# Optimization experiments

Measured on AMD Instinct MI355X. Metric: run time of the kernel, lower is better.

## Reference

```python
import jax, jax.numpy as jnp
import numpy as np

B, T, H, L = 64, 64, 256, 2
INPUT_SIZE = 65
E = INPUT_SIZE - 1  # encoder_in


def setup_inputs() -> dict:
    key = jax.random.key(0)
    ks = jax.random.split(key, 20)
    s = 0.05
    p = {}
    p["input_data"] = jax.random.normal(ks[0], (B, T, INPUT_SIZE), jnp.float32)
    # encoder LSTM (input E -> H, L layers; torch gate order i,f,g,o)
    p["w_ih_e0"] = jax.random.normal(ks[1], (4 * H, E), jnp.float32) * s
    p["w_ih_e1"] = jax.random.normal(ks[2], (L - 1, 4 * H, H), jnp.float32) * s
    p["w_hh_e"] = jax.random.normal(ks[3], (L, 4 * H, H), jnp.float32) * s
    p["b_ih_e"] = jax.random.normal(ks[4], (L, 4 * H), jnp.float32) * s
    p["b_hh_e"] = jax.random.normal(ks[5], (L, 4 * H), jnp.float32) * s
    # decoder LSTM (input H+1 -> H, L layers)
    p["w_ih_d0"] = jax.random.normal(ks[6], (4 * H, H + 1), jnp.float32) * s
    p["w_ih_d1"] = jax.random.normal(ks[7], (L - 1, 4 * H, H), jnp.float32) * s
    p["w_hh_d"] = jax.random.normal(ks[8], (L, 4 * H, H), jnp.float32) * s
    p["b_ih_d"] = jax.random.normal(ks[9], (L, 4 * H), jnp.float32) * s
    p["b_hh_d"] = jax.random.normal(ks[10], (L, 4 * H), jnp.float32) * s
    # encoder attention MLP: Linear(2H+T -> E), Tanh, Linear(E -> 1, no bias)
    p["attn_w1"] = jax.random.normal(ks[11], (E, 2 * H + T), jnp.float32) * s
    p["attn_b1"] = jax.random.normal(ks[12], (E,), jnp.float32) * s
    p["attn_w2"] = jax.random.normal(ks[13], (E,), jnp.float32) * s
    # decoder attention MLP: Linear(3H -> H), Tanh, Linear(H -> 1, no bias)
    p["attnd_w1"] = jax.random.normal(ks[14], (H, 3 * H), jnp.float32) * s
    p["attnd_b1"] = jax.random.normal(ks[15], (H,), jnp.float32) * s
    p["attnd_w2"] = jax.random.normal(ks[16], (H,), jnp.float32) * s
    # output projection: Linear(2H -> 1)
    p["proj_w"] = jax.random.normal(ks[17], (1, 2 * H), jnp.float32) * s
    p["proj_b"] = jax.random.normal(ks[18], (1,), jnp.float32) * s
    return p


def _lstm_step(x, h, c, w_ih0, w_ih_rest, w_hh, b_ih, b_hh):
    """Single-timestep multi-layer LSTM. x: [B, in], h/c: [L, B, H]."""
    hs, cs = [], []
    inp = x
    for l in range(L):
        w_ih = w_ih0 if l == 0 else w_ih_rest[l - 1]
        gates = inp @ w_ih.T + b_ih[l] + h[l] @ w_hh[l].T + b_hh[l]  # [B, 4H]
        i, f, g, o = jnp.split(gates, 4, axis=-1)
        c_new = jax.nn.sigmoid(f) * c[l] + jax.nn.sigmoid(i) * jnp.tanh(g)
        h_new = jax.nn.sigmoid(o) * jnp.tanh(c_new)
        hs.append(h_new)
        cs.append(c_new)
        inp = h_new
    return jnp.stack(hs), jnp.stack(cs)


def reference(input_data, w_ih_e0, w_ih_e1, w_hh_e, b_ih_e, b_hh_e,
              w_ih_d0, w_ih_d1, w_hh_d, b_ih_d, b_hh_d,
              attn_w1, attn_b1, attn_w2, attnd_w1, attnd_b1, attnd_w2,
              proj_w, proj_b):
    input_encoder = input_data[:, :, 1:]             # [B, T, E]
    input_decoder = input_data[:, :, 0]              # [B, T]
    input_permuted = jnp.transpose(input_encoder, (0, 2, 1))  # [B, E, T]

    h0 = jnp.zeros((L, B, H), input_data.dtype)
    c0 = jnp.zeros((L, B, H), input_data.dtype)

    def enc_step(carry, x_t):  # x_t: [B, E]
        h, c = carry
        feat = jnp.concatenate([
            jnp.broadcast_to(h[-1][:, None, :], (B, E, H)),
            jnp.broadcast_to(c[-1][:, None, :], (B, E, H)),
            input_permuted], axis=-1)                # [B, E, 2H+T]
        z = jnp.tanh(feat @ attn_w1.T + attn_b1)     # [B, E, E]
        a = jax.nn.softmax(z @ attn_w2, axis=-1)     # [B, E]
        h, c = _lstm_step(x_t * a, h, c, w_ih_e0, w_ih_e1, w_hh_e, b_ih_e, b_hh_e)
        return (h, c), h[-1]

    _, h_tops = jax.lax.scan(enc_step, (h0, c0), jnp.transpose(input_encoder, (1, 0, 2)))
    h_expanded = jnp.transpose(h_tops, (1, 0, 2))    # [B, T, H]

    def dec_step(carry, d_t):  # d_t: [B]
        h, c = carry
        feat = jnp.concatenate([
            jnp.broadcast_to(h[-1][:, None, :], (B, T, H)),
            jnp.broadcast_to(c[-1][:, None, :], (B, T, H)),
            h_expanded], axis=-1)                    # [B, T, 3H]
        z = jnp.tanh(feat @ attnd_w1.T + attnd_b1)   # [B, T, H]
        a = jax.nn.softmax(z @ attnd_w2, axis=-1)    # [B, T]
        partial = jnp.einsum('bth,bt->bh', h_expanded, a)  # [B, H]
        full = jnp.concatenate([partial, d_t[:, None]], axis=-1)  # [B, H+1]
        h, c = _lstm_step(full, h, c, w_ih_d0, w_ih_d1, w_hh_d, b_ih_d, b_hh_d)
        return (h, c), partial

    (h_d, c_d), partials = jax.lax.scan(dec_step, (h0, c0), input_decoder.T)
    out = jnp.abs(jnp.concatenate([h_d[-1], partials[-1]], axis=-1) @ proj_w.T + proj_b)  # [B, 1]
    return out
```

## Files before the change

### kernel.cpp

```cpp
#include <hip/hip_runtime.h>
#include <hip/hip_fp16.h>
#include <math.h>

#define NT 1024

typedef _Float16 h2v __attribute__((ext_vector_type(2)));
union H8 { uint4 u; h2v h[4]; };

__device__ __forceinline__ float sigf(float x)   { return 1.0f / (1.0f + __expf(-x)); }
__device__ __forceinline__ float tanhf_(float x) { return 1.0f - 2.0f / (1.0f + __expf(2.0f * x)); }
__device__ __forceinline__ float dot4(float4 a, float4 b) {
    return a.x * b.x + a.y * b.y + a.z * b.z + a.w * b.w;
}
__device__ __forceinline__ float red16(float v) {
    v += __shfl_xor(v, 1); v += __shfl_xor(v, 2);
    v += __shfl_xor(v, 4); v += __shfl_xor(v, 8);
    return v;
}
__device__ __forceinline__ float red64(float v) {
    v += __shfl_xor(v, 1);  v += __shfl_xor(v, 2);  v += __shfl_xor(v, 4);
    v += __shfl_xor(v, 8);  v += __shfl_xor(v, 16); v += __shfl_xor(v, 32);
    return v;
}
__device__ __forceinline__ float dot2h(h2v a, h2v b, float c) {
#if __has_builtin(__builtin_amdgcn_fdot2)
    return __builtin_amdgcn_fdot2(a, b, c, false);
#else
    return c + (float)a[0] * (float)b[0] + (float)a[1] * (float)b[1];
#endif
}

__device__ __forceinline__ float exr(const float* p) {
    return __hip_atomic_load(p, __ATOMIC_RELAXED, __HIP_MEMORY_SCOPE_AGENT);
}

__device__ __forceinline__ void xbar(unsigned* ctr, unsigned target) {
    asm volatile("s_waitcnt vmcnt(0)" ::: "memory");
    __syncthreads();
    if (threadIdx.x == 0) {
        __hip_atomic_fetch_add(ctr, 1u, __ATOMIC_RELAXED, __HIP_MEMORY_SCOPE_AGENT);
        while (__hip_atomic_load(ctr, __ATOMIC_RELAXED, __HIP_MEMORY_SCOPE_AGENT) < target)
            __builtin_amdgcn_s_sleep(1);
    }
    __syncthreads();
}

#define OFF_RA   0
#define OFF_RE0  32768
#define OFF_RE1  425984
#define OFF_RDW1 950272
#define OFF_RD0  1081344
#define OFF_RDT  1605632
#define OFF_RD1  1606656
#define TOT_H    2130944

template<int ITERS, bool BIAS, bool DT>
__device__ __forceinline__ void gemv512x(const __half* __restrict__ W,
                                         const __half* __restrict__ act,
                                         const float* __restrict__ bias,
                                         const __half* __restrict__ rdt, float dts,
                                         float* __restrict__ outg,
                                         int jBase, int ljBase) {
    const int lane = threadIdx.x & 63;
    const int q = lane & 15, g = lane >> 4;
    H8 a0, a1, a2, a3;
    a0.u = *(const uint4*)(act + 8 * q);
    a1.u = *(const uint4*)(act + 8 * q + 128);
    a2.u = *(const uint4*)(act + 8 * q + 256);
    a3.u = *(const uint4*)(act + 8 * q + 384);
    #pragma unroll 2
    for (int it = 0; it < ITERS; ++it) {
        const int j = jBase + it * 4 + g;
        const uint4* wp = (const uint4*)(W + ((size_t)j << 9) + 32 * q);
        H8 w0, w1, w2, w3;
        w0.u = wp[0]; w1.u = wp[1]; w2.u = wp[2]; w3.u = wp[3];
        float s0 = 0.f, s1 = 0.f;
        #pragma unroll
        for (int i = 0; i < 4; ++i) {
            s0 = dot2h(w0.h[i], a0.h[i], s0);
            s1 = dot2h(w1.h[i], a1.h[i], s1);
            s0 = dot2h(w2.h[i], a2.h[i], s0);
            s1 = dot2h(w3.h[i], a3.h[i], s1);
        }
        float s = s0 + s1;
        s += __shfl_xor(s, 1); s += __shfl_xor(s, 2);
        s += __shfl_xor(s, 4); s += __shfl_xor(s, 8);
        if (q == 0) {
            if (DT) s += dts * (float)rdt[j];
            outg[ljBase + it * 4 + g] = BIAS ? s + bias[j] : s;
        }
    }
}

template<int ITERS>
__device__ __forceinline__ void gemv384x(const __half* __restrict__ W,
                                         const __half* __restrict__ act,
                                         const float* __restrict__ bias,
                                         float* __restrict__ outg,
                                         int jBase, int ljBase) {
    const int lane = threadIdx.x & 63;
    const int q = lane & 15, g = lane >> 4;
    H8 a0, a1, a2;
    a0.u = *(const uint4*)(act + 8 * q);
    a1.u = *(const uint4*)(act + 8 * q + 128);
    a2.u = *(const uint4*)(act + 8 * q + 256);
    #pragma unroll 2
    for (int it = 0; it < ITERS; ++it) {
        const int j = jBase + it * 4 + g;
        const uint4* wp = (const uint4*)(W + (size_t)j * 384 + 24 * q);
        H8 w0, w1, w2;
        w0.u = wp[0]; w1.u = wp[1]; w2.u = wp[2];
        float s0 = 0.f, s1 = 0.f;
        #pragma unroll
        for (int i = 0; i < 4; ++i) {
            s0 = dot2h(w0.h[i], a0.h[i], s0);
            s1 = dot2h(w1.h[i], a1.h[i], s1);
            s0 = dot2h(w2.h[i], a2.h[i], s0);
        }
        float s = s0 + s1;
        s += __shfl_xor(s, 1); s += __shfl_xor(s, 2);
        s += __shfl_xor(s, 4); s += __shfl_xor(s, 8);
        if (q == 0) outg[ljBase + it * 4 + g] = s + bias[j];
    }
}

#define M_HEXP  0
#define M_XET   16384
#define M_GSL   20736
#define M_HCT   20992
#define M_TMP   21248
#define M_SCORE 21312
#define M_AS    21376
#define M_C0    21440
#define M_C1    21504
#define M_HC1F  21568
#define M_DECIN 21824
#define M_PARTF 21888
#define M_BE0   22144
#define M_BE1   23168
#define M_BD0   24192
#define M_BD1   25216
#define M_AHC   26240
#define M_AE0   26496
#define M_AHH   26688
#define M_AD0   26944
#define M_RDT   27200
#define M_TOT   27712

extern "C" __global__ void __launch_bounds__(NT)
attn_lstm_v6(const float* __restrict__ inp,  const __half* __restrict__ wsh,
             float* __restrict__ h0x, float* __restrict__ h1x,
             float* __restrict__ hcx, unsigned* __restrict__ barc,
             const float* __restrict__ bihe, const float* __restrict__ bhhe,
             const float* __restrict__ bihd, const float* __restrict__ bhhd,
             const float* __restrict__ aw1,  const float* __restrict__ ab1,
             const float* __restrict__ aw2,
             const float* __restrict__ dw1,  const float* __restrict__ db1,
             const float* __restrict__ dw2,
             const float* __restrict__ pw,   const float* __restrict__ pb,
             float* __restrict__ out)
{
    extern __shared__ __align__(16) float sm[];
    float* hexp   = sm + M_HEXP;
    float* xeT    = sm + M_XET;
    float* gsl    = sm + M_GSL;
    float* hctL   = sm + M_HCT;
    float* tmp64  = sm + M_TMP;
    float* scoreS = sm + M_SCORE;
    float* aS     = sm + M_AS;
    float* c0L    = sm + M_C0;
    float* c1L    = sm + M_C1;
    float* hc1f   = sm + M_HC1F;
    float* decin  = sm + M_DECIN;
    float* partF  = sm + M_PARTF;
    float* bE0    = sm + M_BE0;
    float* bE1    = sm + M_BE1;
    float* bD0    = sm + M_BD0;
    float* bD1    = sm + M_BD1;
    __half* aHC   = (__half*)(sm + M_AHC);
    __half* aE0   = (__half*)(sm + M_AE0);
    __half* aHH   = (__half*)(sm + M_AHH);
    __half* aD0   = (__half*)(sm + M_AD0);
    __half* rdtL  = (__half*)(sm + M_RDT);

    const __half* RA   = wsh + OFF_RA;
    const __half* RE0  = wsh + OFF_RE0;
    const __half* RE1  = wsh + OFF_RE1;
    const __half* RDW1 = wsh + OFF_RDW1;
    const __half* RD0  = wsh + OFF_RD0;
    const __half* RD1  = wsh + OFF_RD1;

    const int tid = threadIdx.x;
    const int b   = blockIdx.x >> 2;
    const int co  = blockIdx.x & 3;
    const int w   = tid >> 6;
    unsigned* ctr = barc + (b << 4);
    unsigned  ph  = 0;

    if (tid < 64) { c0L[tid] = 0.f; c1L[tid] = 0.f; }
    for (int i = tid; i < 960; i += NT) sm[M_AHC + i] = 0.0f;
    if (tid < 512) sm[M_RDT + tid] = ((const float*)(wsh + OFF_RDT))[tid];
    {
        int j = tid;
        bE0[j] = bihe[j]        + bhhe[j];
        bE1[j] = bihe[1024 + j] + bhhe[1024 + j];
        bD0[j] = bihd[j]        + bhhd[j];
        bD1[j] = bihd[1024 + j] + bhhd[1024 + j];
    }
    const float* ib = inp + b * (64 * 65);
    for (int i = tid; i < 4096; i += NT) {
        int t = i & 63, e = i >> 6;
        xeT[e * 68 + t] = ib[t * 65 + 1 + e];
    }
    if (tid < 64) decin[tid] = ib[tid * 65];
    __syncthreads();

    const int g16 = tid >> 4, q16 = tid & 15;
    const int gg = w >> 2, cb = (w & 3) << 4;
    const int jB  = gg * 256 + co * 64 + cb;
    const int ljB = gg * 64 + cb;

    float Preg[4], w2r[4];
    #pragma unroll
    for (int jj = 0; jj < 4; ++jj) {
        int j = q16 + 16 * jj;
        w2r[jj] = aw2[j];
        float acc = ab1[j];
        const float4* w4 = (const float4*)(aw1 + j * 576 + 512);
        const float4* x4 = (const float4*)(xeT + g16 * 68);
        #pragma unroll 4
        for (int k = 0; k < 16; ++k) acc += dot4(w4[k], x4[k]);
        Preg[jj] = acc;
    }

    for (int t = 0; t < 64; ++t) {
        const int p = t & 1;
        float* h0b = h0x + p * 16384 + b * 256;
        float* h1b = h1x + p * 32768 + b * 512;
        gemv512x<1, false, false>(RA, aHC, nullptr, nullptr, 0.f, hctL, w * 4, w * 4);
        __syncthreads();
        {
            float s = 0.f;
            #pragma unroll
            for (int jj = 0; jj < 4; ++jj)
                s += tanhf_(Preg[jj] + hctL[q16 + 16 * jj]) * w2r[jj];
            s = red16(s);
            if (q16 == 0) scoreS[g16] = s;
        }
        __syncthreads();
        if (tid < 64) {
            float v = scoreS[tid], m = v;
            #pragma unroll
            for (int d = 1; d < 64; d <<= 1) m = fmaxf(m, __shfl_xor(m, d));
            float ex = __expf(v - m), s = ex;
            #pragma unroll
            for (int d = 1; d < 64; d <<= 1) s += __shfl_xor(s, d);
            aE0[tid] = __float2half((ex / s) * xeT[tid * 68 + t]);
        }
        __syncthreads();
        gemv384x<4>(RE0, aE0, bE0, gsl, jB, ljB);
        __syncthreads();
        if (tid < 64) {
            float cn = sigf(gsl[64 + tid]) * c0L[tid] + sigf(gsl[tid]) * tanhf_(gsl[128 + tid]);
            float hn = sigf(gsl[192 + tid]) * tanhf_(cn);
            c0L[tid] = cn;
            atomicExch(&h0b[co * 64 + tid], hn);
        }
        xbar(ctr, ++ph * 4u);
        if (tid < 256) {
            __half hh = __float2half(exr(&h0b[tid]));
            aE0[64 + tid] = hh; aHH[tid] = hh;
        }
        __syncthreads();
        gemv512x<4, true, false>(RE1, aHH, bE1, nullptr, 0.f, gsl, jB, ljB);
        __syncthreads();
        if (tid < 64) {
            float cn = sigf(gsl[64 + tid]) * c1L[tid] + sigf(gsl[tid]) * tanhf_(gsl[128 + tid]);
            float hn = sigf(gsl[192 + tid]) * tanhf_(cn);
            c1L[tid] = cn;
            atomicExch(&h1b[co * 64 + tid], hn);
            atomicExch(&h1b[256 + co * 64 + tid], cn);
        }
        xbar(ctr, ++ph * 4u);
        if (tid < 512) {
            float v = exr(&h1b[tid]);
            __half hh = __float2half(v);
            aHC[tid] = hh;
            if (tid < 256) { aHH[256 + tid] = hh; hexp[t * 256 + tid] = v; }
        }
        __syncthreads();
    }

    if (tid < 64) { c0L[tid] = 0.f; c1L[tid] = 0.f; }
    for (int i = tid; i < 960; i += NT) sm[M_AHC + i] = 0.0f;
    __syncthreads();
    float Pdreg[16], w2dr[16];
    #pragma unroll
    for (int jj = 0; jj < 16; ++jj) {
        int j = q16 + 16 * jj;
        w2dr[jj] = dw2[j];
        float acc = db1[j];
        const float4* w4 = (const float4*)(dw1 + j * 768 + 512);
        const float4* x4 = (const float4*)(hexp + g16 * 256);
        #pragma unroll 4
        for (int k = 0; k < 64; ++k) acc += dot4(w4[k], x4[k]);
        Pdreg[jj] = acc;
    }
    __syncthreads();

    const int j4 = tid >> 2, q4 = tid & 3;
    for (int t = 0; t < 64; ++t) {
        const int p = t & 1;
        float* h0b = h0x + p * 16384 + b * 256;
        float* h1b = h1x + p * 32768 + b * 512;
        float* hcb = hcx + p * 16384 + b * 256;
        gemv512x<1, false, false>(RDW1, aHC, nullptr, nullptr, 0.f, tmp64,
                                  co * 64 + w * 4, w * 4);
        __syncthreads();
        if (tid < 64) atomicExch(&hcb[co * 64 + tid], tmp64[tid]);
        xbar(ctr, ++ph * 4u);
        if (tid < 256) hctL[tid] = exr(&hcb[tid]);
        __syncthreads();
        {
            float s = 0.f;
            #pragma unroll
            for (int jj = 0; jj < 16; ++jj)
                s += tanhf_(Pdreg[jj] + hctL[q16 + 16 * jj]) * w2dr[jj];
            s = red16(s);
            if (q16 == 0) scoreS[g16] = s;
        }
        __syncthreads();
        if (tid < 64) {
            float v = scoreS[tid], m = v;
            #pragma unroll
            for (int d = 1; d < 64; d <<= 1) m = fmaxf(m, __shfl_xor(m, d));
            float ex = __expf(v - m), s = ex;
            #pragma unroll
            for (int d = 1; d < 64; d <<= 1) s += __shfl_xor(s, d);
            aS[tid] = ex / s;
        }
        __syncthreads();
        {
            float acc = 0.f;
            #pragma unroll 4
            for (int i = 0; i < 16; ++i) {
                int tt = q4 + 4 * i;
                acc += hexp[tt * 256 + j4] * aS[tt];
            }
            acc += __shfl_xor(acc, 1);
            acc += __shfl_xor(acc, 2);
            if (q4 == 0) { aD0[j4] = __float2half(acc); partF[j4] = acc; }
        }
        __syncthreads();
        gemv512x<4, true, true>(RD0, aD0, bD0, rdtL, decin[t], gsl, jB, ljB);
        __syncthreads();
        if (tid < 64) {
            float cn = sigf(gsl[64 + tid]) * c0L[tid] + sigf(gsl[tid]) * tanhf_(gsl[128 + tid]);
            float hn = sigf(gsl[192 + tid]) * tanhf_(cn);
            c0L[tid] = cn;
            atomicExch(&h0b[co * 64 + tid], hn);
        }
        xbar(ctr, ++ph * 4u);
        if (tid < 256) {
            __half hh = __float2half(exr(&h0b[tid]));
            aD0[256 + tid] = hh; aHH[tid] = hh;
        }
        __syncthreads();
        gemv512x<4, true, false>(RD1, aHH, bD1, nullptr, 0.f, gsl, jB, ljB);
        __syncthreads();
        if (tid < 64) {
            float cn = sigf(gsl[64 + tid]) * c1L[tid] + sigf(gsl[tid]) * tanhf_(gsl[128 + tid]);
            float hn = sigf(gsl[192 + tid]) * tanhf_(cn);
            c1L[tid] = cn;
            atomicExch(&h1b[co * 64 + tid], hn);
            atomicExch(&h1b[256 + co * 64 + tid], cn);
        }
        xbar(ctr, ++ph * 4u);
        if (tid < 512) {
            float v = exr(&h1b[tid]);
            __half hh = __float2half(v);
            aHC[tid] = hh;
            if (tid < 256) { aHH[256 + tid] = hh; hc1f[tid] = v; }
        }
        __syncthreads();
    }

    if (co == 0 && tid < 64) {
        float acc = 0.f;
        #pragma unroll
        for (int i = 0; i < 8; ++i) {
            int k = tid + 64 * i;
            float v = (k < 256) ? hc1f[k] : partF[k - 256];
            acc += v * pw[k];
        }
        acc = red64(acc);
        if (tid == 0) out[b] = fabsf(acc + pb[0]);
    }
}

#define L_HEXP   0
#define L_XET    16384
#define L_GSL    20736
#define L_HCT    21760
#define L_SCORE  22016
#define L_AS     22080
#define L_C0     22144
#define L_HC1F   22400
#define L_DECIN  22912
#define L_PARTF  22976
#define L_BE0    23232
#define L_BE1    24256
#define L_BD0    25280
#define L_BD1    26304
#define L_AHC    27328
#define L_AE0    27584
#define L_AHH    27776
#define L_AD0    28032
#define L_RDT    28288
#define L_TOT    28800

extern "C" __global__ void __launch_bounds__(NT)
attn_lstm_v5(const float* __restrict__ inp,  const __half* __restrict__ wsh,
             const float* __restrict__ bihe, const float* __restrict__ bhhe,
             const float* __restrict__ bihd, const float* __restrict__ bhhd,
             const float* __restrict__ aw1,  const float* __restrict__ ab1,
             const float* __restrict__ aw2,
             const float* __restrict__ dw1,  const float* __restrict__ db1,
             const float* __restrict__ dw2,
             const float* __restrict__ pw,   const float* __restrict__ pb,
             float* __restrict__ out)
{
    extern __shared__ __align__(16) float sm[];
    float* hexp   = sm + L_HEXP;
    float* xeT    = sm + L_XET;
    float* gsl    = sm + L_GSL;
    float* hctL   = sm + L_HCT;
    float* scoreS = sm + L_SCORE;
    float* aS     = sm + L_AS;
    float* c0L    = sm + L_C0;
    float* hc1f   = sm + L_HC1F;
    float* decin  = sm + L_DECIN;
    float* partF  = sm + L_PARTF;
    float* bE0    = sm + L_BE0;
    float* bE1    = sm + L_BE1;
    float* bD0    = sm + L_BD0;
    float* bD1    = sm + L_BD1;
    __half* aHC   = (__half*)(sm + L_AHC);
    __half* aE0   = (__half*)(sm + L_AE0);
    __half* aHH   = (__half*)(sm + L_AHH);
    __half* aD0   = (__half*)(sm + L_AD0);
    __half* rdtL  = (__half*)(sm + L_RDT);

    const __half* RA   = wsh + OFF_RA;
    const __half* RE0  = wsh + OFF_RE0;
    const __half* RE1  = wsh + OFF_RE1;
    const __half* RDW1 = wsh + OFF_RDW1;
    const __half* RD0  = wsh + OFF_RD0;
    const __half* RD1  = wsh + OFF_RD1;

    const int b   = blockIdx.x;
    const int tid = threadIdx.x;
    const int w   = tid >> 6;

    for (int i = tid; i < (L_BE0 - L_C0); i += NT) sm[L_C0 + i] = 0.0f;
    for (int i = tid; i < (L_RDT - L_AHC); i += NT) sm[L_AHC + i] = 0.0f;
    if (tid < 512) sm[L_RDT + tid] = ((const float*)(wsh + OFF_RDT))[tid];
    {
        int j = tid;
        bE0[j] = bihe[j]        + bhhe[j];
        bE1[j] = bihe[1024 + j] + bhhe[1024 + j];
        bD0[j] = bihd[j]        + bhhd[j];
        bD1[j] = bihd[1024 + j] + bhhd[1024 + j];
    }
    const float* ib = inp + b * (64 * 65);
    for (int i = tid; i < 4096; i += NT) {
        int t = i & 63, e = i >> 6;
        xeT[e * 68 + t] = ib[t * 65 + 1 + e];
    }
    if (tid < 64) decin[tid] = ib[tid * 65];
    __syncthreads();

    const int g16 = tid >> 4, q16 = tid & 15;

    float Preg[4], w2r[4];
    #pragma unroll
    for (int jj = 0; jj < 4; ++jj) {
        int j = q16 + 16 * jj;
        w2r[jj] = aw2[j];
        float acc = ab1[j];
        const float4* w4 = (const float4*)(aw1 + j * 576 + 512);
        const float4* x4 = (const float4*)(xeT + g16 * 68);
        #pragma unroll 4
        for (int k = 0; k < 16; ++k) acc += dot4(w4[k], x4[k]);
        Preg[jj] = acc;
    }

    for (int t = 0; t < 64; ++t) {
        gemv512x<1, false, false>(RA, aHC, nullptr, nullptr, 0.f, hctL, w * 4, w * 4);
        __syncthreads();
        {
            float s = 0.f;
            #pragma unroll
            for (int jj = 0; jj < 4; ++jj)
                s += tanhf_(Preg[jj] + hctL[q16 + 16 * jj]) * w2r[jj];
            s = red16(s);
            if (q16 == 0) scoreS[g16] = s;
        }
        __syncthreads();
        if (tid < 64) {
            float v = scoreS[tid], m = v;
            #pragma unroll
            for (int d = 1; d < 64; d <<= 1) m = fmaxf(m, __shfl_xor(m, d));
            float ex = __expf(v - m), s = ex;
            #pragma unroll
            for (int d = 1; d < 64; d <<= 1) s += __shfl_xor(s, d);
            aE0[tid] = __float2half((ex / s) * xeT[tid * 68 + t]);
        }
        __syncthreads();
        gemv384x<16>(RE0, aE0, bE0, gsl, w * 64, w * 64);
        __syncthreads();
        if (tid < 256) {
            float cn = sigf(gsl[256 + tid]) * c0L[tid] + sigf(gsl[tid]) * tanhf_(gsl[512 + tid]);
            float hn = sigf(gsl[768 + tid]) * tanhf_(cn);
            c0L[tid] = cn;
            __half hh = __float2half(hn);
            aE0[64 + tid] = hh; aHH[tid] = hh;
        }
        __syncthreads();
        gemv512x<16, true, false>(RE1, aHH, bE1, nullptr, 0.f, gsl, w * 64, w * 64);
        __syncthreads();
        if (tid < 256) {
            float cp = hc1f[256 + tid];
            float cn = sigf(gsl[256 + tid]) * cp + sigf(gsl[tid]) * tanhf_(gsl[512 + tid]);
            float hn = sigf(gsl[768 + tid]) * tanhf_(cn);
            hc1f[tid] = hn; hc1f[256 + tid] = cn;
            __half hh = __float2half(hn);
            aHC[tid] = hh; aHC[256 + tid] = __float2half(cn);
            aHH[256 + tid] = hh;
            hexp[t * 256 + tid] = hn;
        }
        __syncthreads();
    }

    if (tid < 256) { c0L[tid] = 0.0f; hc1f[tid] = 0.0f; hc1f[256 + tid] = 0.0f; }
    for (int i = tid; i < (L_RDT - L_AHC); i += NT) sm[L_AHC + i] = 0.0f;
    __syncthreads();
    float Pdreg[16], w2dr[16];
    #pragma unroll
    for (int jj = 0; jj < 16; ++jj) {
        int j = q16 + 16 * jj;
        w2dr[jj] = dw2[j];
        float acc = db1[j];
        const float4* w4 = (const float4*)(dw1 + j * 768 + 512);
        const float4* x4 = (const float4*)(hexp + g16 * 256);
        #pragma unroll 4
        for (int k = 0; k < 64; ++k) acc += dot4(w4[k], x4[k]);
        Pdreg[jj] = acc;
    }
    __syncthreads();

    const int j4 = tid >> 2, q4 = tid & 3;
    for (int t = 0; t < 64; ++t) {
        gemv512x<4, false, false>(RDW1, aHC, nullptr, nullptr, 0.f, hctL, w * 16, w * 16);
        __syncthreads();
        {
            float s = 0.f;
            #pragma unroll
            for (int jj = 0; jj < 16; ++jj)
                s += tanhf_(Pdreg[jj] + hctL[q16 + 16 * jj]) * w2dr[jj];
            s = red16(s);
            if (q16 == 0) scoreS[g16] = s;
        }
        __syncthreads();
        if (tid < 64) {
            float v = scoreS[tid], m = v;
            #pragma unroll
            for (int d = 1; d < 64; d <<= 1) m = fmaxf(m, __shfl_xor(m, d));
            float ex = __expf(v - m), s = ex;
            #pragma unroll
            for (int d = 1; d < 64; d <<= 1) s += __shfl_xor(s, d);
            aS[tid] = ex / s;
        }
        __syncthreads();
        {
            float acc = 0.f;
            #pragma unroll 4
            for (int i = 0; i < 16; ++i) {
                int tt = q4 + 4 * i;
                acc += hexp[tt * 256 + j4] * aS[tt];
            }
            acc += __shfl_xor(acc, 1);
            acc += __shfl_xor(acc, 2);
            if (q4 == 0) { aD0[j4] = __float2half(acc); partF[j4] = acc; }
        }
        __syncthreads();
        gemv512x<16, true, true>(RD0, aD0, bD0, rdtL, decin[t], gsl, w * 64, w * 64);
        __syncthreads();
        if (tid < 256) {
            float cn = sigf(gsl[256 + tid]) * c0L[tid] + sigf(gsl[tid]) * tanhf_(gsl[512 + tid]);
            float hn = sigf(gsl[768 + tid]) * tanhf_(cn);
            c0L[tid] = cn;
            __half hh = __float2half(hn);
            aD0[256 + tid] = hh; aHH[tid] = hh;
        }
        __syncthreads();
        gemv512x<16, true, false>(RD1, aHH, bD1, nullptr, 0.f, gsl, w * 64, w * 64);
        __syncthreads();
        if (tid < 256) {
            float cp = hc1f[256 + tid];
            float cn = sigf(gsl[256 + tid]) * cp + sigf(gsl[tid]) * tanhf_(gsl[512 + tid]);
            float hn = sigf(gsl[768 + tid]) * tanhf_(cn);
            hc1f[tid] = hn; hc1f[256 + tid] = cn;
            __half hh = __float2half(hn);
            aHC[tid] = hh; aHC[256 + tid] = __float2half(cn);
            aHH[256 + tid] = hh;
        }
        __syncthreads();
    }

    if (tid < 64) {
        float acc = 0.f;
        #pragma unroll
        for (int i = 0; i < 8; ++i) {
            int k = tid + 64 * i;
            float v = (k < 256) ? hc1f[k] : partF[k - 256];
            acc += v * pw[k];
        }
        acc = red64(acc);
        if (tid == 0) out[b] = fabsf(acc + pb[0]);
    }
}

extern "C" __global__ void repack16b(const float* __restrict__ wihe0,
                                     const float* __restrict__ wihe1,
                                     const float* __restrict__ whhe,
                                     const float* __restrict__ wihd0,
                                     const float* __restrict__ wihd1,
                                     const float* __restrict__ whhd,
                                     const float* __restrict__ aw1,
                                     const float* __restrict__ dw1,
                                     __half* __restrict__ ws) {
    int idx = blockIdx.x * blockDim.x + threadIdx.x;
    if (idx >= TOT_H) return;
    int o = idx; float v;
    if (o < 32768) {
        int j = o >> 9, p = o & 511;
        int q = p >> 5, r = p & 31, c = r >> 3, e = r & 7;
        int k = 8 * q + 128 * c + e;
        v = aw1[j * 576 + k];
        ws[OFF_RA + o] = __float2half_rn(v); return;
    }
    o -= 32768;
    if (o < 393216) {
        int j = o / 384, p = o - j * 384;
        int q = p / 24, r = p - q * 24, c = r >> 3, e = r & 7;
        int k = 8 * q + 128 * c + e;
        v = (k < 64) ? wihe0[j * 64 + k] : (k < 320 ? whhe[j * 256 + (k - 64)] : 0.0f);
        ws[OFF_RE0 + o] = __float2half_rn(v); return;
    }
    o -= 393216;
    if (o < 524288) {
        int j = o >> 9, p = o & 511;
        int q = p >> 5, r = p & 31, c = r >> 3, e = r & 7;
        int k = 8 * q + 128 * c + e;
        v = (k < 256) ? wihe1[j * 256 + k] : whhe[262144 + j * 256 + (k - 256)];
        ws[OFF_RE1 + o] = __float2half_rn(v); return;
    }
    o -= 524288;
    if (o < 131072) {
        int j = o >> 9, p = o & 511;
        int q = p >> 5, r = p & 31, c = r >> 3, e = r & 7;
        int k = 8 * q + 128 * c + e;
        v = dw1[j * 768 + k];
        ws[OFF_RDW1 + o] = __float2half_rn(v); return;
    }
    o -= 131072;
    if (o < 524288) {
        int j = o >> 9, p = o & 511;
        int q = p >> 5, r = p & 31, c = r >> 3, e = r & 7;
        int k = 8 * q + 128 * c + e;
        v = (k < 256) ? wihd0[j * 257 + k] : whhd[j * 256 + (k - 256)];
        ws[OFF_RD0 + o] = __float2half_rn(v); return;
    }
    o -= 524288;
    if (o < 1024) {
        v = wihd0[o * 257 + 256];
        ws[OFF_RDT + o] = __float2half_rn(v); return;
    }
    o -= 1024;
    {
        int j = o >> 9, p = o & 511;
        int q = p >> 5, r = p & 31, c = r >> 3, e = r & 7;
        int k = 8 * q + 128 * c + e;
        v = (k < 256) ? wihd1[j * 256 + k] : whhd[262144 + j * 256 + (k - 256)];
        ws[OFF_RD1 + o] = __float2half_rn(v);
    }
}

extern "C" void kernel_launch(void* const* d_in, const int* in_sizes, int n_in,
                              void* d_out, int out_size, void* d_ws, size_t ws_size,
                              hipStream_t stream) {
    const float* inp   = (const float*)d_in[0];
    const float* wihe0 = (const float*)d_in[1];
    const float* wihe1 = (const float*)d_in[2];
    const float* whhe  = (const float*)d_in[3];
    const float* bihe  = (const float*)d_in[4];
    const float* bhhe  = (const float*)d_in[5];
    const float* wihd0 = (const float*)d_in[6];
    const float* wihd1 = (const float*)d_in[7];
    const float* whhd  = (const float*)d_in[8];
    const float* bihd  = (const float*)d_in[9];
    const float* bhhd  = (const float*)d_in[10];
    const float* aw1   = (const float*)d_in[11];
    const float* ab1   = (const float*)d_in[12];
    const float* aw2   = (const float*)d_in[13];
    const float* dw1   = (const float*)d_in[14];
    const float* db1   = (const float*)d_in[15];
    const float* dw2   = (const float*)d_in[16];
    const float* pw    = (const float*)d_in[17];
    const float* pb    = (const float*)d_in[18];
    float* out = (float*)d_out;

    const size_t EX0 = TOT_H / 2;
    const size_t H0X = EX0;
    const size_t H1X = EX0 + 32768;
    const size_t HCX = EX0 + 98304;
    const size_t CTR = EX0 + 131072;
    const size_t NEED6 = (CTR + 1024) * sizeof(float);

    if (ws_size >= NEED6) {
        float* ws32 = (float*)d_ws;
        __half* wsh = (__half*)d_ws;
        hipMemsetAsync((char*)d_ws + CTR * sizeof(float), 0, 4096, stream);
        repack16b<<<(TOT_H + 255) / 256, 256, 0, stream>>>(
            wihe0, wihe1, whhe, wihd0, wihd1, whhd, aw1, dw1, wsh);
        const int smem = M_TOT * 4;
        hipFuncSetAttribute((const void*)attn_lstm_v6,
                            hipFuncAttributeMaxDynamicSharedMemorySize, smem);
        attn_lstm_v6<<<256, NT, smem, stream>>>(
            inp, wsh, ws32 + H0X, ws32 + H1X, ws32 + HCX,
            (unsigned*)(ws32 + CTR),
            bihe, bhhe, bihd, bhhd,
            aw1, ab1, aw2, dw1, db1, dw2, pw, pb, out);
        return;
    }

    if (ws_size >= (size_t)TOT_H * sizeof(__half)) {
        __half* wsh = (__half*)d_ws;
        repack16b<<<(TOT_H + 255) / 256, 256, 0, stream>>>(
            wihe0, wihe1, whhe, wihd0, wihd1, whhd, aw1, dw1, wsh);
        const int smem = L_TOT * 4;
        hipFuncSetAttribute((const void*)attn_lstm_v5,
                            hipFuncAttributeMaxDynamicSharedMemorySize, smem);
        attn_lstm_v5<<<64, NT, smem, stream>>>(
            inp, wsh, bihe, bhhe, bihd, bhhd,
            aw1, ab1, aw2, dw1, db1, dw2, pw, pb, out);
    }
}
```

Baseline: 2.253 ms.

## Split each batch row across eight 512-thread blocks and precompute decoder attention projection

Replaces the v6 kernel (4 cooperating 1024-thread blocks per batch row) with v8, which uses 8 cooperating 512-thread blocks per row. Each block owns 32 hidden units across the four gates. The time-invariant part of the decoder attention MLP (W1 applied to the encoder outputs) is precomputed once into fp16 shared memory, so each decoder step only computes the h/c projection and a tanh-sum. Encoder outputs are kept in fp16 in LDS, and the barrier is split into signal and wait halves. The changes aim to spread the per-step GEMV weight traffic over more CUs and remove redundant attention work, at the cost of more inter-block synchronisation per step and extra fp16 rounding of the attention scores.

Result: faster. 2.168 ms (-3.8%).

```diff
diff --git a/kernel.cpp b/kernel.cpp
--- a/kernel.cpp
+++ b/kernel.cpp
@@ -2,7 +2,8 @@
 #include <hip/hip_fp16.h>
 #include <math.h>
 
-#define NT 1024
+#define NT8 512
+#define NT  1024
 
 typedef _Float16 h2v __attribute__((ext_vector_type(2)));
 union H8 { uint4 u; h2v h[4]; };
@@ -15,6 +16,10 @@
 __device__ __forceinline__ float red16(float v) {
     v += __shfl_xor(v, 1); v += __shfl_xor(v, 2);
     v += __shfl_xor(v, 4); v += __shfl_xor(v, 8);
+    return v;
+}
+__device__ __forceinline__ float red8(float v) {
+    v += __shfl_xor(v, 1); v += __shfl_xor(v, 2); v += __shfl_xor(v, 4);
     return v;
 }
 __device__ __forceinline__ float red64(float v) {
@@ -33,12 +38,14 @@
 __device__ __forceinline__ float exr(const float* p) {
     return __hip_atomic_load(p, __ATOMIC_RELAXED, __HIP_MEMORY_SCOPE_AGENT);
 }
-
-__device__ __forceinline__ void xbar(unsigned* ctr, unsigned target) {
-    asm volatile("s_waitcnt vmcnt(0)" ::: "memory");
-    __syncthreads();
+__device__ __forceinline__ void xsig(unsigned* ctr) {
     if (threadIdx.x == 0) {
+        asm volatile("s_waitcnt vmcnt(0)" ::: "memory");
         __hip_atomic_fetch_add(ctr, 1u, __ATOMIC_RELAXED, __HIP_MEMORY_SCOPE_AGENT);
+    }
+}
+__device__ __forceinline__ void xwait(unsigned* ctr, unsigned target) {
+    if (threadIdx.x == 0) {
         while (__hip_atomic_load(ctr, __ATOMIC_RELAXED, __HIP_MEMORY_SCOPE_AGENT) < target)
             __builtin_amdgcn_s_sleep(1);
     }
@@ -52,15 +59,496 @@
 #define OFF_RD0  1081344
 #define OFF_RDT  1605632
 #define OFF_RD1  1606656
-#define TOT_H    2130944
+#define OFF_RPD  2130944
+#define TOT_H2   2196480
 
 template<int ITERS, bool BIAS, bool DT>
-__device__ __forceinline__ void gemv512x(const __half* __restrict__ W,
+__device__ __forceinline__ void gemvS512(const __half* __restrict__ W,
+                                         const __half* __restrict__ act,
+                                         const float* __restrict__ biasF,
+                                         const __half* __restrict__ rdtH, float dts,
+                                         float* __restrict__ outg, int coB) {
+    const int lane = threadIdx.x & 63;
+    const int q = lane & 15, g = lane >> 4;
+    const int w = threadIdx.x >> 6;
+    H8 a0, a1, a2, a3;
+    a0.u = *(const uint4*)(act + 8 * q);
+    a1.u = *(const uint4*)(act + 8 * q + 128);
+    a2.u = *(const uint4*)(act + 8 * q + 256);
+    a3.u = *(const uint4*)(act + 8 * q + 384);
+    #pragma unroll 2
+    for (int it = 0; it < ITERS; ++it) {
+        const int l = w * 16 + it * 4 + g;
+        const int j = ((l & 0x60) << 3) + coB + (l & 31);
+        const uint4* wp = (const uint4*)(W + ((size_t)j << 9) + 32 * q);
+        H8 w0, w1, w2, w3;
+        w0.u = wp[0]; w1.u = wp[1]; w2.u = wp[2]; w3.u = wp[3];
+        float s0 = 0.f, s1 = 0.f;
+        #pragma unroll
+        for (int i = 0; i < 4; ++i) {
+            s0 = dot2h(w0.h[i], a0.h[i], s0);
+            s1 = dot2h(w1.h[i], a1.h[i], s1);
+            s0 = dot2h(w2.h[i], a2.h[i], s0);
+            s1 = dot2h(w3.h[i], a3.h[i], s1);
+        }
+        float s = red16(s0 + s1);
+        if (q == 0) {
+            if (DT) s += dts * (float)rdtH[l];
+            outg[l] = BIAS ? s + biasF[l] : s;
+        }
+    }
+}
+
+template<int ITERS>
+__device__ __forceinline__ void gemvS384(const __half* __restrict__ W,
+                                         const __half* __restrict__ act,
+                                         const float* __restrict__ biasF,
+                                         float* __restrict__ outg, int coB) {
+    const int lane = threadIdx.x & 63;
+    const int q = lane & 15, g = lane >> 4;
+    const int w = threadIdx.x >> 6;
+    H8 a0, a1, a2;
+    a0.u = *(const uint4*)(act + 8 * q);
+    a1.u = *(const uint4*)(act + 8 * q + 128);
+    a2.u = *(const uint4*)(act + 8 * q + 256);
+    #pragma unroll 2
+    for (int it = 0; it < ITERS; ++it) {
+        const int l = w * 16 + it * 4 + g;
+        const int j = ((l & 0x60) << 3) + coB + (l & 31);
+        const h2v* hp = (const h2v*)(W + (size_t)j * 384 + 24 * q);
+        float s0 = 0.f, s1 = 0.f;
+        #pragma unroll
+        for (int i = 0; i < 4; ++i) s0 = dot2h(hp[i],     a0.h[i], s0);
+        #pragma unroll
+        for (int i = 0; i < 4; ++i) s1 = dot2h(hp[4 + i], a1.h[i], s1);
+        #pragma unroll
+        for (int i = 0; i < 4; ++i) s0 = dot2h(hp[8 + i], a2.h[i], s0);
+        float s = red16(s0 + s1);
+        if (q == 0) outg[l] = s + biasF[l];
+    }
+}
+
+__device__ __forceinline__ void gemvE1(const __half* __restrict__ W,
+                                       const __half* __restrict__ act,
+                                       float* __restrict__ outg) {
+    const int lane = threadIdx.x & 63;
+    const int q = lane & 15, g = lane >> 4;
+    const int w = threadIdx.x >> 6;
+    H8 a0, a1, a2, a3;
+    a0.u = *(const uint4*)(act + 8 * q);
+    a1.u = *(const uint4*)(act + 8 * q + 128);
+    a2.u = *(const uint4*)(act + 8 * q + 256);
+    a3.u = *(const uint4*)(act + 8 * q + 384);
+    #pragma unroll
+    for (int it = 0; it < 2; ++it) {
+        const int j = w * 8 + it * 4 + g;
+        const uint4* wp = (const uint4*)(W + ((size_t)j << 9) + 32 * q);
+        H8 w0, w1, w2, w3;
+        w0.u = wp[0]; w1.u = wp[1]; w2.u = wp[2]; w3.u = wp[3];
+        float s0 = 0.f, s1 = 0.f;
+        #pragma unroll
+        for (int i = 0; i < 4; ++i) {
+            s0 = dot2h(w0.h[i], a0.h[i], s0);
+            s1 = dot2h(w1.h[i], a1.h[i], s1);
+            s0 = dot2h(w2.h[i], a2.h[i], s0);
+            s1 = dot2h(w3.h[i], a3.h[i], s1);
+        }
+        float s = red16(s0 + s1);
+        if (q == 0) outg[j] = s;
+    }
+}
+
+#define V8_HEXP  0
+#define V8_R     8192
+#define V8_GSL   16384
+#define V8_HCT   16512
+#define V8_SCORE 16768
+#define V8_AS    16832
+#define V8_C0    16896
+#define V8_C1    16928
+#define V8_HC1F  16960
+#define V8_DECIN 17216
+#define V8_PARTF 17280
+#define V8_BE0   17536
+#define V8_BE1   17664
+#define V8_BD0   17792
+#define V8_BD1   17920
+#define V8_AHC   18048
+#define V8_AE0   18304
+#define V8_AHH   18496
+#define V8_AD0   18752
+#define V8_RDT   19008
+#define V8_W2D   19072
+#define V8_TMP   19328
+#define V8_TOT   19360
+
+extern "C" __global__ void __launch_bounds__(NT8)
+attn_lstm_v8(const float* __restrict__ inp,  const __half* __restrict__ wsh,
+             float* __restrict__ h0x, float* __restrict__ h1x,
+             float* __restrict__ hcx, unsigned* __restrict__ barc,
+             const float* __restrict__ bihe, const float* __restrict__ bhhe,
+             const float* __restrict__ bihd, const float* __restrict__ bhhd,
+             const float* __restrict__ aw1,  const float* __restrict__ ab1,
+             const float* __restrict__ aw2,  const float* __restrict__ db1,
+             const float* __restrict__ dw2,
+             const float* __restrict__ pw,   const float* __restrict__ pb,
+             float* __restrict__ out)
+{
+    extern __shared__ __align__(16) float sm[];
+    __half* hexp16 = (__half*)(sm + V8_HEXP);
+    float*  xeT    = sm + V8_R;
+    __half* PdL16  = (__half*)(sm + V8_R);
+    float* gsl    = sm + V8_GSL;
+    float* hctL   = sm + V8_HCT;
+    float* scoreS = sm + V8_SCORE;
+    float* aS     = sm + V8_AS;
+    float* c0L    = sm + V8_C0;
+    float* c1L    = sm + V8_C1;
+    float* hc1f   = sm + V8_HC1F;
+    float* decin  = sm + V8_DECIN;
+    float* partF  = sm + V8_PARTF;
+    float* bE0f   = sm + V8_BE0;
+    float* bE1f   = sm + V8_BE1;
+    float* bD0f   = sm + V8_BD0;
+    float* bD1f   = sm + V8_BD1;
+    __half* aHC   = (__half*)(sm + V8_AHC);
+    __half* aE0   = (__half*)(sm + V8_AE0);
+    __half* aHH   = (__half*)(sm + V8_AHH);
+    __half* aD0   = (__half*)(sm + V8_AD0);
+    __half* rdtH  = (__half*)(sm + V8_RDT);
+    float* w2dL   = sm + V8_W2D;
+    float* tmp32  = sm + V8_TMP;
+
+    const __half* RA   = wsh + OFF_RA;
+    const __half* RE0  = wsh + OFF_RE0;
+    const __half* RE1  = wsh + OFF_RE1;
+    const __half* RDW1 = wsh + OFF_RDW1;
+    const __half* RD0  = wsh + OFF_RD0;
+    const __half* RD1  = wsh + OFF_RD1;
+    const __half* RPD  = wsh + OFF_RPD;
+
+    const int tid = threadIdx.x;
+    const int b   = blockIdx.x >> 3;
+    const int co  = blockIdx.x & 7;
+    const int coB = co * 32;
+    const int w   = tid >> 6;
+    const int lane = tid & 63;
+    const int q16 = lane & 15, g4 = lane >> 4;
+    unsigned* ctr = barc + (b << 4);
+    unsigned  ph  = 0;
+
+    for (int i = tid; i < V8_TOT - V8_GSL; i += NT8) sm[V8_GSL + i] = 0.0f;
+    const float* ib = inp + b * (64 * 65);
+    for (int i = tid; i < 4096; i += NT8) {
+        int t = i & 63, e = i >> 6;
+        xeT[e * 68 + t] = ib[t * 65 + 1 + e];
+    }
+    __syncthreads();
+    if (tid < 128) {
+        int l = tid;
+        int j = ((l & 0x60) << 3) + coB + (l & 31);
+        bE0f[l] = bihe[j]        + bhhe[j];
+        bE1f[l] = bihe[1024 + j] + bhhe[1024 + j];
+        bD0f[l] = bihd[j]        + bhhd[j];
+        bD1f[l] = bihd[1024 + j] + bhhd[1024 + j];
+        rdtH[l] = wsh[OFF_RDT + j];
+    }
+    if (tid < 64) decin[tid] = ib[tid * 65];
+    if (tid < 256) w2dL[tid] = dw2[tid];
+    __syncthreads();
+
+    const int e8 = tid >> 3, q8 = tid & 7;
+    float Preg[8], w2r[8];
+    #pragma unroll
+    for (int jj = 0; jj < 8; ++jj) {
+        int j = q8 + 8 * jj;
+        w2r[jj] = aw2[j];
+        float acc = ab1[j];
+        const float4* w4 = (const float4*)(aw1 + j * 576 + 512);
+        const float4* x4 = (const float4*)(xeT + e8 * 68);
+        #pragma unroll 4
+        for (int k = 0; k < 16; ++k) acc += dot4(w4[k], x4[k]);
+        Preg[jj] = acc;
+    }
+
+    for (int t = 0; t < 64; ++t) {
+        const int p = t & 1;
+        float* h0b = h0x + p * 16384 + b * 256;
+        float* h1b = h1x + p * 32768 + b * 512;
+        gemvE1(RA, aHC, hctL);
+        __syncthreads();
+        {
+            float s = 0.f;
+            #pragma unroll
+            for (int jj = 0; jj < 8; ++jj)
+                s += tanhf_(Preg[jj] + hctL[q8 + 8 * jj]) * w2r[jj];
+            s = red8(s);
+            if (q8 == 0) scoreS[e8] = s;
+        }
+        __syncthreads();
+        if (tid < 64) {
+            float v = scoreS[tid], m = v;
+            #pragma unroll
+            for (int d = 1; d < 64; d <<= 1) m = fmaxf(m, __shfl_xor(m, d));
+            float ex = __expf(v - m), s = ex;
+            #pragma unroll
+            for (int d = 1; d < 64; d <<= 1) s += __shfl_xor(s, d);
+            aE0[tid] = __float2half((ex / s) * xeT[tid * 68 + t]);
+        }
+        __syncthreads();
+        gemvS384<4>(RE0, aE0, bE0f, gsl, coB);
+        __syncthreads();
+        if (tid < 32) {
+            float cn = sigf(gsl[32 + tid]) * c0L[tid] + sigf(gsl[tid]) * tanhf_(gsl[64 + tid]);
+            float hn = sigf(gsl[96 + tid]) * tanhf_(cn);
+            c0L[tid] = cn;
+            atomicExch(&h0b[coB + tid], hn);
+        }
+        xsig(ctr); ++ph;
+        xwait(ctr, ph * 8u);
+        if (tid < 256) {
+            __half hh = __float2half(exr(&h0b[tid]));
+            aE0[64 + tid] = hh; aHH[tid] = hh;
+        }
+        __syncthreads();
+        gemvS512<4, true, false>(RE1, aHH, bE1f, nullptr, 0.f, gsl, coB);
+        __syncthreads();
+        if (tid < 32) {
+            float cn = sigf(gsl[32 + tid]) * c1L[tid] + sigf(gsl[tid]) * tanhf_(gsl[64 + tid]);
+            float hn = sigf(gsl[96 + tid]) * tanhf_(cn);
+            c1L[tid] = cn;
+            atomicExch(&h1b[coB + tid], hn);
+            atomicExch(&h1b[256 + coB + tid], cn);
+        }
+        xsig(ctr); ++ph;
+        xwait(ctr, ph * 8u);
+        if (tid < 512) {
+            float v = exr(&h1b[tid]);
+            __half hh = __float2half(v);
+            aHC[tid] = hh;
+            if (tid < 256) { aHH[256 + tid] = hh; hexp16[t * 256 + tid] = hh; }
+        }
+        __syncthreads();
+    }
+
+    if (tid < 32) { c0L[tid] = 0.f; c1L[tid] = 0.f; }
+    for (int i = tid; i < 960; i += NT8) sm[V8_AHC + i] = 0.0f;
+    __syncthreads();
+    {
+        #pragma unroll 1
+        for (int it = 0; it < 8; ++it) {
+            const int j = it * 32 + w * 4 + g4;
+            const h2v* wp = (const h2v*)(RPD + ((size_t)j << 8) + 16 * q16);
+            h2v w0 = wp[0], w1 = wp[1], w2 = wp[2], w3 = wp[3];
+            h2v w4 = wp[4], w5 = wp[5], w6 = wp[6], w7 = wp[7];
+            float dbj = db1[j];
+            #pragma unroll 2
+            for (int tp = 0; tp < 64; ++tp) {
+                const h2v* xp = (const h2v*)(hexp16 + tp * 256 + 8 * q16);
+                const h2v* yp = (const h2v*)(hexp16 + tp * 256 + 8 * q16 + 128);
+                float s = 0.f;
+                s = dot2h(w0, xp[0], s); s = dot2h(w1, xp[1], s);
+                s = dot2h(w2, xp[2], s); s = dot2h(w3, xp[3], s);
+                s = dot2h(w4, yp[0], s); s = dot2h(w5, yp[1], s);
+                s = dot2h(w6, yp[2], s); s = dot2h(w7, yp[3], s);
+                s = red16(s);
+                if (q16 == 0) PdL16[tp * 256 + j] = __float2half(s + dbj);
+            }
+        }
+    }
+    __syncthreads();
+
+    for (int t = 0; t < 64; ++t) {
+        const int p = t & 1;
+        float* h0b = h0x + p * 16384 + b * 256;
+        float* h1b = h1x + p * 32768 + b * 512;
+        float* hcb = hcx + p * 16384 + b * 256;
+        {
+            const int l = w * 4 + g4;
+            const int j = coB + l;
+            H8 a0, a1, a2, a3;
+            a0.u = *(const uint4*)((const __half*)aHC + 8 * q16);
+            a1.u = *(const uint4*)((const __half*)aHC + 8 * q16 + 128);
+            a2.u = *(const uint4*)((const __half*)aHC + 8 * q16 + 256);
+            a3.u = *(const uint4*)((const __half*)aHC + 8 * q16 + 384);
+            const uint4* wp = (const uint4*)(RDW1 + ((size_t)j << 9) + 32 * q16);
+            H8 w0, w1, w2, w3;
+            w0.u = wp[0]; w1.u = wp[1]; w2.u = wp[2]; w3.u = wp[3];
+            float s0 = 0.f, s1 = 0.f;
+            #pragma unroll
+            for (int i = 0; i < 4; ++i) {
+                s0 = dot2h(w0.h[i], a0.h[i], s0);
+                s1 = dot2h(w1.h[i], a1.h[i], s1);
+                s0 = dot2h(w2.h[i], a2.h[i], s0);
+                s1 = dot2h(w3.h[i], a3.h[i], s1);
+            }
+            float s = red16(s0 + s1);
+            if (q16 == 0) tmp32[l] = s;
+        }
+        __syncthreads();
+        if (tid < 32) atomicExch(&hcb[coB + tid], tmp32[tid]);
+        xsig(ctr); ++ph;
+        xwait(ctr, ph * 8u);
+        if (tid < 256) hctL[tid] = exr(&hcb[tid]);
+        __syncthreads();
+        {
+            float s = 0.f;
+            #pragma unroll 8
+            for (int jj = 0; jj < 32; ++jj) {
+                int j = q8 + 8 * jj;
+                s += tanhf_((float)PdL16[e8 * 256 + j] + hctL[j]) * w2dL[j];
+            }
+            s = red8(s);
+            if (q8 == 0) scoreS[e8] = s;
+        }
+        __syncthreads();
+        if (tid < 64) {
+            float v = scoreS[tid], m = v;
+            #pragma unroll
+            for (int d = 1; d < 64; d <<= 1) m = fmaxf(m, __shfl_xor(m, d));
+            float ex = __expf(v - m), s = ex;
+            #pragma unroll
+            for (int d = 1; d < 64; d <<= 1) s += __shfl_xor(s, d);
+            aS[tid] = ex / s;
+        }
+        __syncthreads();
+        if (tid < 256) {
+            float acc = 0.f;
+            #pragma unroll 8
+            for (int tt = 0; tt < 64; ++tt)
+                acc += (float)hexp16[tt * 256 + tid] * aS[tt];
+            partF[tid] = acc;
+            aD0[tid] = __float2half(acc);
+        }
+        __syncthreads();
+        gemvS512<4, true, true>(RD0, aD0, bD0f, rdtH, decin[t], gsl, coB);
+        __syncthreads();
+        if (tid < 32) {
+            float cn = sigf(gsl[32 + tid]) * c0L[tid] + sigf(gsl[tid]) * tanhf_(gsl[64 + tid]);
+            float hn = sigf(gsl[96 + tid]) * tanhf_(cn);
+            c0L[tid] = cn;
+            atomicExch(&h0b[coB + tid], hn);
+        }
+        xsig(ctr); ++ph;
+        xwait(ctr, ph * 8u);
+        if (tid < 256) {
+            __half hh = __float2half(exr(&h0b[tid]));
+            aD0[256 + tid] = hh; aHH[tid] = hh;
+        }
+        __syncthreads();
+        gemvS512<4, true, false>(RD1, aHH, bD1f, nullptr, 0.f, gsl, coB);
+        __syncthreads();
+        if (tid < 32) {
+            float cn = sigf(gsl[32 + tid]) * c1L[tid] + sigf(gsl[tid]) * tanhf_(gsl[64 + tid]);
+            float hn = sigf(gsl[96 + tid]) * tanhf_(cn);
+            c1L[tid] = cn;
+            atomicExch(&h1b[coB + tid], hn);
+            atomicExch(&h1b[256 + coB + tid], cn);
+        }
+        xsig(ctr); ++ph;
+        xwait(ctr, ph * 8u);
+        if (tid < 512) {
+            float v = exr(&h1b[tid]);
+            __half hh = __float2half(v);
+            aHC[tid] = hh;
+            if (tid < 256) { aHH[256 + tid] = hh; hc1f[tid] = v; }
+        }
+        __syncthreads();
+    }
+
+    if (co == 0 && tid < 64) {
+        float acc = 0.f;
+        #pragma unroll
+        for (int i = 0; i < 8; ++i) {
+            int k = tid + 64 * i;
+            float v = (k < 256) ? hc1f[k] : partF[k - 256];
+            acc += v * pw[k];
+        }
+        acc = red64(acc);
+        if (tid == 0) out[b] = fabsf(acc + pb[0]);
+    }
+}
+
+extern "C" __global__ void repack16c(const float* __restrict__ wihe0,
+                                     const float* __restrict__ wihe1,
+                                     const float* __restrict__ whhe,
+                                     const float* __restrict__ wihd0,
+                                     const float* __restrict__ wihd1,
+                                     const float* __restrict__ whhd,
+                                     const float* __restrict__ aw1,
+                                     const float* __restrict__ dw1,
+                                     __half* __restrict__ ws) {
+    int idx = blockIdx.x * blockDim.x + threadIdx.x;
+    if (idx >= TOT_H2) return;
+    int o = idx; float v;
+    if (o < 32768) {
+        int j = o >> 9, p = o & 511;
+        int q = p >> 5, r = p & 31, c = r >> 3, e = r & 7;
+        int k = 8 * q + 128 * c + e;
+        v = aw1[j * 576 + k];
+        ws[OFF_RA + o] = __float2half_rn(v); return;
+    }
+    o -= 32768;
+    if (o < 393216) {
+        int j = o / 384, p = o - j * 384;
+        int q = p / 24, r = p - q * 24, c = r >> 3, e = r & 7;
+        int k = 8 * q + 128 * c + e;
+        v = (k < 64) ? wihe0[j * 64 + k] : (k < 320 ? whhe[j * 256 + (k - 64)] : 0.0f);
+        ws[OFF_RE0 + o] = __float2half_rn(v); return;
+    }
+    o -= 393216;
+    if (o < 524288) {
+        int j = o >> 9, p = o & 511;
+        int q = p >> 5, r = p & 31, c = r >> 3, e = r & 7;
+        int k = 8 * q + 128 * c + e;
+        v = (k < 256) ? wihe1[j * 256 + k] : whhe[262144 + j * 256 + (k - 256)];
+        ws[OFF_RE1 + o] = __float2half_rn(v); return;
+    }
+    o -= 524288;
+    if (o < 131072) {
+        int j = o >> 9, p = o & 511;
+        int q = p >> 5, r = p & 31, c = r >> 3, e = r & 7;
+        int k = 8 * q + 128 * c + e;
+        v = dw1[j * 768 + k];
+        ws[OFF_RDW1 + o] = __float2half_rn(v); return;
+    }
+    o -= 131072;
+    if (o < 524288) {
+        int j = o >> 9, p = o & 511;
+        int q = p >> 5, r = p & 31, c = r >> 3, e = r & 7;
+        int k = 8 * q + 128 * c + e;
+        v = (k < 256) ? wihd0[j * 257 + k] : whhd[j * 256 + (k - 256)];
+        ws[OFF_RD0 + o] = __float2half_rn(v); return;
+    }
+    o -= 524288;
+    if (o < 1024) {
+        v = wihd0[o * 257 + 256];
+        ws[OFF_RDT + o] = __float2half_rn(v); return;
+    }
+    o -= 1024;
+    if (o < 524288) {
+        int j = o >> 9, p = o & 511;
+        int q = p >> 5, r = p & 31, c = r >> 3, e = r & 7;
+        int k = 8 * q + 128 * c + e;
+        v = (k < 256) ? wihd1[j * 256 + k] : whhd[262144 + j * 256 + (k - 256)];
+        ws[OFF_RD1 + o] = __float2half_rn(v); return;
+    }
+    o -= 524288;
+    {
+        int j = o >> 8, p = o & 255;
+        int q = p >> 4, r = p & 15, c = r >> 3, e = r & 7;
+        int k = 8 * q + 128 * c + e;
+        v = dw1[j * 768 + 512 + k];
+        ws[OFF_RPD + o] = __float2half_rn(v);
+    }
+}
+
+template<int ITERS, bool BIAS, bool DT>
+__device__ __forceinline__ void gemv512f(const __half* __restrict__ W,
                                          const __half* __restrict__ act,
                                          const float* __restrict__ bias,
                                          const __half* __restrict__ rdt, float dts,
-                                         float* __restrict__ outg,
-                                         int jBase, int ljBase) {
+                                         float* __restrict__ outg, int rowBase) {
     const int lane = threadIdx.x & 63;
     const int q = lane & 15, g = lane >> 4;
     H8 a0, a1, a2, a3;
@@ -70,7 +558,7 @@
     a3.u = *(const uint4*)(act + 8 * q + 384);
     #pragma unroll 2
     for (int it = 0; it < ITERS; ++it) {
-        const int j = jBase + it * 4 + g;
+        const int j = rowBase + it * 4 + g;
         const uint4* wp = (const uint4*)(W + ((size_t)j << 9) + 32 * q);
         H8 w0, w1, w2, w3;
         w0.u = wp[0]; w1.u = wp[1]; w2.u = wp[2]; w3.u = wp[3];
@@ -82,22 +570,18 @@
             s0 = dot2h(w2.h[i], a2.h[i], s0);
             s1 = dot2h(w3.h[i], a3.h[i], s1);
         }
-        float s = s0 + s1;
-        s += __shfl_xor(s, 1); s += __shfl_xor(s, 2);
-        s += __shfl_xor(s, 4); s += __shfl_xor(s, 8);
+        float s = red16(s0 + s1);
         if (q == 0) {
             if (DT) s += dts * (float)rdt[j];
-            outg[ljBase + it * 4 + g] = BIAS ? s + bias[j] : s;
-        }
-    }
-}
-
+            outg[j] = BIAS ? s + bias[j] : s;
+        }
+    }
+}
 template<int ITERS>
-__device__ __forceinline__ void gemv384x(const __half* __restrict__ W,
+__device__ __forceinline__ void gemv384f(const __half* __restrict__ W,
                                          const __half* __restrict__ act,
                                          const float* __restrict__ bias,
-                                         float* __restrict__ outg,
-                                         int jBase, int ljBase) {
+                                         float* __restrict__ outg, int rowBase) {
     const int lane = threadIdx.x & 63;
     const int q = lane & 15, g = lane >> 4;
     H8 a0, a1, a2;
@@ -106,295 +590,17 @@
     a2.u = *(const uint4*)(act + 8 * q + 256);
     #pragma unroll 2
     for (int it = 0; it < ITERS; ++it) {
-        const int j = jBase + it * 4 + g;
-        const uint4* wp = (const uint4*)(W + (size_t)j * 384 + 24 * q);
-        H8 w0, w1, w2;
-        w0.u = wp[0]; w1.u = wp[1]; w2.u = wp[2];
+        const int j = rowBase + it * 4 + g;
+        const h2v* hp = (const h2v*)(W + (size_t)j * 384 + 24 * q);
         float s0 = 0.f, s1 = 0.f;
         #pragma unroll
-        for (int i = 0; i < 4; ++i) {
-            s0 = dot2h(w0.h[i], a0.h[i], s0);
-            s1 = dot2h(w1.h[i], a1.h[i], s1);
-            s0 = dot2h(w2.h[i], a2.h[i], s0);
-        }
-        float s = s0 + s1;
-        s += __shfl_xor(s, 1); s += __shfl_xor(s, 2);
-        s += __shfl_xor(s, 4); s += __shfl_xor(s, 8);
-        if (q == 0) outg[ljBase + it * 4 + g] = s + bias[j];
-    }
-}
-
-#define M_HEXP  0
-#define M_XET   16384
-#define M_GSL   20736
-#define M_HCT   20992
-#define M_TMP   21248
-#define M_SCORE 21312
-#define M_AS    21376
-#define M_C0    21440
-#define M_C1    21504
-#define M_HC1F  21568
-#define M_DECIN 21824
-#define M_PARTF 21888
-#define M_BE0   22144
-#define M_BE1   23168
-#define M_BD0   24192
-#define M_BD1   25216
-#define M_AHC   26240
-#define M_AE0   26496
-#define M_AHH   26688
-#define M_AD0   26944
-#define M_RDT   27200
-#define M_TOT   27712
-
-extern "C" __global__ void __launch_bounds__(NT)
-attn_lstm_v6(const float* __restrict__ inp,  const __half* __restrict__ wsh,
-             float* __restrict__ h0x, float* __restrict__ h1x,
-             float* __restrict__ hcx, unsigned* __restrict__ barc,
-             const float* __restrict__ bihe, const float* __restrict__ bhhe,
-             const float* __restrict__ bihd, const float* __restrict__ bhhd,
-             const float* __restrict__ aw1,  const float* __restrict__ ab1,
-             const float* __restrict__ aw2,
-             const float* __restrict__ dw1,  const float* __restrict__ db1,
-             const float* __restrict__ dw2,
-             const float* __restrict__ pw,   const float* __restrict__ pb,
-             float* __restrict__ out)
-{
-    extern __shared__ __align__(16) float sm[];
-    float* hexp   = sm + M_HEXP;
-    float* xeT    = sm + M_XET;
-    float* gsl    = sm + M_GSL;
-    float* hctL   = sm + M_HCT;
-    float* tmp64  = sm + M_TMP;
-    float* scoreS = sm + M_SCORE;
-    float* aS     = sm + M_AS;
-    float* c0L    = sm + M_C0;
-    float* c1L    = sm + M_C1;
-    float* hc1f   = sm + M_HC1F;
-    float* decin  = sm + M_DECIN;
-    float* partF  = sm + M_PARTF;
-    float* bE0    = sm + M_BE0;
-    float* bE1    = sm + M_BE1;
-    float* bD0    = sm + M_BD0;
-    float* bD1    = sm + M_BD1;
-    __half* aHC   = (__half*)(sm + M_AHC);
-    __half* aE0   = (__half*)(sm + M_AE0);
-    __half* aHH   = (__half*)(sm + M_AHH);
-    __half* aD0   = (__half*)(sm + M_AD0);
-    __half* rdtL  = (__half*)(sm + M_RDT);
-
-    const __half* RA   = wsh + OFF_RA;
-    const __half* RE0  = wsh + OFF_RE0;
-    const __half* RE1  = wsh + OFF_RE1;
-    const __half* RDW1 = wsh + OFF_RDW1;
-    const __half* RD0  = wsh + OFF_RD0;
-    const __half* RD1  = wsh + OFF_RD1;
-
-    const int tid = threadIdx.x;
-    const int b   = blockIdx.x >> 2;
-    const int co  = blockIdx.x & 3;
-    const int w   = tid >> 6;
-    unsigned* ctr = barc + (b << 4);
-    unsigned  ph  = 0;
-
-    if (tid < 64) { c0L[tid] = 0.f; c1L[tid] = 0.f; }
-    for (int i = tid; i < 960; i += NT) sm[M_AHC + i] = 0.0f;
-    if (tid < 512) sm[M_RDT + tid] = ((const float*)(wsh + OFF_RDT))[tid];
-    {
-        int j = tid;
-        bE0[j] = bihe[j]        + bhhe[j];
-        bE1[j] = bihe[1024 + j] + bhhe[1024 + j];
-        bD0[j] = bihd[j]        + bhhd[j];
-        bD1[j] = bihd[1024 + j] + bhhd[1024 + j];
-    }
-    const float* ib = inp + b * (64 * 65);
-    for (int i = tid; i < 4096; i += NT) {
-        int t = i & 63, e = i >> 6;
-        xeT[e * 68 + t] = ib[t * 65 + 1 + e];
-    }
-    if (tid < 64) decin[tid] = ib[tid * 65];
-    __syncthreads();
-
-    const int g16 = tid >> 4, q16 = tid & 15;
-    const int gg = w >> 2, cb = (w & 3) << 4;
-    const int jB  = gg * 256 + co * 64 + cb;
-    const int ljB = gg * 64 + cb;
-
-    float Preg[4], w2r[4];
-    #pragma unroll
-    for (int jj = 0; jj < 4; ++jj) {
-        int j = q16 + 16 * jj;
-        w2r[jj] = aw2[j];
-        float acc = ab1[j];
-        const float4* w4 = (const float4*)(aw1 + j * 576 + 512);
-        const float4* x4 = (const float4*)(xeT + g16 * 68);
-        #pragma unroll 4
-        for (int k = 0; k < 16; ++k) acc += dot4(w4[k], x4[k]);
-        Preg[jj] = acc;
-    }
-
-    for (int t = 0; t < 64; ++t) {
-        const int p = t & 1;
-        float* h0b = h0x + p * 16384 + b * 256;
-        float* h1b = h1x + p * 32768 + b * 512;
-        gemv512x<1, false, false>(RA, aHC, nullptr, nullptr, 0.f, hctL, w * 4, w * 4);
-        __syncthreads();
-        {
-            float s = 0.f;
-            #pragma unroll
-            for (int jj = 0; jj < 4; ++jj)
-                s += tanhf_(Preg[jj] + hctL[q16 + 16 * jj]) * w2r[jj];
-            s = red16(s);
-            if (q16 == 0) scoreS[g16] = s;
-        }
-        __syncthreads();
-        if (tid < 64) {
-            float v = scoreS[tid], m = v;
-            #pragma unroll
-            for (int d = 1; d < 64; d <<= 1) m = fmaxf(m, __shfl_xor(m, d));
-            float ex = __expf(v - m), s = ex;
-            #pragma unroll
-            for (int d = 1; d < 64; d <<= 1) s += __shfl_xor(s, d);
-            aE0[tid] = __float2half((ex / s) * xeT[tid * 68 + t]);
-        }
-        __syncthreads();
-        gemv384x<4>(RE0, aE0, bE0, gsl, jB, ljB);
-        __syncthreads();
-        if (tid < 64) {
-            float cn = sigf(gsl[64 + tid]) * c0L[tid] + sigf(gsl[tid]) * tanhf_(gsl[128 + tid]);
-            float hn = sigf(gsl[192 + tid]) * tanhf_(cn);
-            c0L[tid] = cn;
-            atomicExch(&h0b[co * 64 + tid], hn);
-        }
-        xbar(ctr, ++ph * 4u);
-        if (tid < 256) {
-            __half hh = __float2half(exr(&h0b[tid]));
-            aE0[64 + tid] = hh; aHH[tid] = hh;
-        }
-        __syncthreads();
-        gemv512x<4, true, false>(RE1, aHH, bE1, nullptr, 0.f, gsl, jB, ljB);
-        __syncthreads();
-        if (tid < 64) {
-            float cn = sigf(gsl[64 + tid]) * c1L[tid] + sigf(gsl[tid]) * tanhf_(gsl[128 + tid]);
-            float hn = sigf(gsl[192 + tid]) * tanhf_(cn);
-            c1L[tid] = cn;
-            atomicExch(&h1b[co * 64 + tid], hn);
-            atomicExch(&h1b[256 + co * 64 + tid], cn);
-        }
-        xbar(ctr, ++ph * 4u);
-        if (tid < 512) {
-            float v = exr(&h1b[tid]);
-            __half hh = __float2half(v);
-            aHC[tid] = hh;
-            if (tid < 256) { aHH[256 + tid] = hh; hexp[t * 256 + tid] = v; }
-        }
-        __syncthreads();
-    }
-
-    if (tid < 64) { c0L[tid] = 0.f; c1L[tid] = 0.f; }
-    for (int i = tid; i < 960; i += NT) sm[M_AHC + i] = 0.0f;
-    __syncthreads();
-    float Pdreg[16], w2dr[16];
-    #pragma unroll
-    for (int jj = 0; jj < 16; ++jj) {
-        int j = q16 + 16 * jj;
-        w2dr[jj] = dw2[j];
-        float acc = db1[j];
-        const float4* w4 = (const float4*)(dw1 + j * 768 + 512);
-        const float4* x4 = (const float4*)(hexp + g16 * 256);
-        #pragma unroll 4
-        for (int k = 0; k < 64; ++k) acc += dot4(w4[k], x4[k]);
-        Pdreg[jj] = acc;
-    }
-    __syncthreads();
-
-    const int j4 = tid >> 2, q4 = tid & 3;
-    for (int t = 0; t < 64; ++t) {
-        const int p = t & 1;
-        float* h0b = h0x + p * 16384 + b * 256;
-        float* h1b = h1x + p * 32768 + b * 512;
-        float* hcb = hcx + p * 16384 + b * 256;
-        gemv512x<1, false, false>(RDW1, aHC, nullptr, nullptr, 0.f, tmp64,
-                                  co * 64 + w * 4, w * 4);
-        __syncthreads();
-        if (tid < 64) atomicExch(&hcb[co * 64 + tid], tmp64[tid]);
-        xbar(ctr, ++ph * 4u);
-        if (tid < 256) hctL[tid] = exr(&hcb[tid]);
-        __syncthreads();
-        {
-            float s = 0.f;
-            #pragma unroll
-            for (int jj = 0; jj < 16; ++jj)
-                s += tanhf_(Pdreg[jj] + hctL[q16 + 16 * jj]) * w2dr[jj];
-            s = red16(s);
-            if (q16 == 0) scoreS[g16] = s;
-        }
-        __syncthreads();
-        if (tid < 64) {
-            float v = scoreS[tid], m = v;
-            #pragma unroll
-            for (int d = 1; d < 64; d <<= 1) m = fmaxf(m, __shfl_xor(m, d));
-            float ex = __expf(v - m), s = ex;
-            #pragma unroll
-            for (int d = 1; d < 64; d <<= 1) s += __shfl_xor(s, d);
-            aS[tid] = ex / s;
-        }
-        __syncthreads();
-        {
-            float acc = 0.f;
-            #pragma unroll 4
-            for (int i = 0; i < 16; ++i) {
-                int tt = q4 + 4 * i;
-                acc += hexp[tt * 256 + j4] * aS[tt];
-            }
-            acc += __shfl_xor(acc, 1);
-            acc += __shfl_xor(acc, 2);
-            if (q4 == 0) { aD0[j4] = __float2half(acc); partF[j4] = acc; }
-        }
-        __syncthreads();
-        gemv512x<4, true, true>(RD0, aD0, bD0, rdtL, decin[t], gsl, jB, ljB);
-        __syncthreads();
-        if (tid < 64) {
-            float cn = sigf(gsl[64 + tid]) * c0L[tid] + sigf(gsl[tid]) * tanhf_(gsl[128 + tid]);
-            float hn = sigf(gsl[192 + tid]) * tanhf_(cn);
-            c0L[tid] = cn;
-            atomicExch(&h0b[co * 64 + tid], hn);
-        }
-        xbar(ctr, ++ph * 4u);
-        if (tid < 256) {
-            __half hh = __float2half(exr(&h0b[tid]));
-            aD0[256 + tid] = hh; aHH[tid] = hh;
-        }
-        __syncthreads();
-        gemv512x<4, true, false>(RD1, aHH, bD1, nullptr, 0.f, gsl, jB, ljB);
-        __syncthreads();
-        if (tid < 64) {
-            float cn = sigf(gsl[64 + tid]) * c1L[tid] + sigf(gsl[tid]) * tanhf_(gsl[128 + tid]);
-            float hn = sigf(gsl[192 + tid]) * tanhf_(cn);
-            c1L[tid] = cn;
-            atomicExch(&h1b[co * 64 + tid], hn);
-            atomicExch(&h1b[256 + co * 64 + tid], cn);
-        }
-        xbar(ctr, ++ph * 4u);
-        if (tid < 512) {
-            float v = exr(&h1b[tid]);
-            __half hh = __float2half(v);
-            aHC[tid] = hh;
-            if (tid < 256) { aHH[256 + tid] = hh; hc1f[tid] = v; }
-        }
-        __syncthreads();
-    }
-
-    if (co == 0 && tid < 64) {
-        float acc = 0.f;
-        #pragma unroll
-        for (int i = 0; i < 8; ++i) {
-            int k = tid + 64 * i;
-            float v = (k < 256) ? hc1f[k] : partF[k - 256];
-            acc += v * pw[k];
-        }
-        acc = red64(acc);
-        if (tid == 0) out[b] = fabsf(acc + pb[0]);
+        for (int i = 0; i < 4; ++i) s0 = dot2h(hp[i],     a0.h[i], s0);
+        #pragma unroll
+        for (int i = 0; i < 4; ++i) s1 = dot2h(hp[4 + i], a1.h[i], s1);
+        #pragma unroll
+        for (int i = 0; i < 4; ++i) s0 = dot2h(hp[8 + i], a2.h[i], s0);
+        float s = red16(s0 + s1);
+        if (q == 0) outg[j] = s + bias[j];
     }
 }
 
@@ -496,7 +702,7 @@
     }
 
     for (int t = 0; t < 64; ++t) {
-        gemv512x<1, false, false>(RA, aHC, nullptr, nullptr, 0.f, hctL, w * 4, w * 4);
+        gemv512f<1, false, false>(RA, aHC, nullptr, nullptr, 0.f, hctL, w * 4);
         __syncthreads();
         {
             float s = 0.f;
@@ -517,7 +723,7 @@
             aE0[tid] = __float2half((ex / s) * xeT[tid * 68 + t]);
         }
         __syncthreads();
-        gemv384x<16>(RE0, aE0, bE0, gsl, w * 64, w * 64);
+        gemv384f<16>(RE0, aE0, bE0, gsl, w * 64);
         __syncthreads();
         if (tid < 256) {
             float cn = sigf(gsl[256 + tid]) * c0L[tid] + sigf(gsl[tid]) * tanhf_(gsl[512 + tid]);
@@ -527,7 +733,7 @@
             aE0[64 + tid] = hh; aHH[tid] = hh;
         }
         __syncthreads();
-        gemv512x<16, true, false>(RE1, aHH, bE1, nullptr, 0.f, gsl, w * 64, w * 64);
+        gemv512f<16, true, false>(RE1, aHH, bE1, nullptr, 0.f, gsl, w * 64);
         __syncthreads();
         if (tid < 256) {
             float cp = hc1f[256 + tid];
@@ -561,7 +767,7 @@
 
     const int j4 = tid >> 2, q4 = tid & 3;
     for (int t = 0; t < 64; ++t) {
-        gemv512x<4, false, false>(RDW1, aHC, nullptr, nullptr, 0.f, hctL, w * 16, w * 16);
+        gemv512f<4, false, false>(RDW1, aHC, nullptr, nullptr, 0.f, hctL, w * 16);
         __syncthreads();
         {
             float s = 0.f;
@@ -594,7 +800,7 @@
             if (q4 == 0) { aD0[j4] = __float2half(acc); partF[j4] = acc; }
         }
         __syncthreads();
-        gemv512x<16, true, true>(RD0, aD0, bD0, rdtL, decin[t], gsl, w * 64, w * 64);
+        gemv512f<16, true, true>(RD0, aD0, bD0, rdtL, decin[t], gsl, w * 64);
         __syncthreads();
         if (tid < 256) {
             float cn = sigf(gsl[256 + tid]) * c0L[tid] + sigf(gsl[tid]) * tanhf_(gsl[512 + tid]);
@@ -604,7 +810,7 @@
             aD0[256 + tid] = hh; aHH[tid] = hh;
         }
         __syncthreads();
-        gemv512x<16, true, false>(RD1, aHH, bD1, nullptr, 0.f, gsl, w * 64, w * 64);
+        gemv512f<16, true, false>(RD1, aHH, bD1, nullptr, 0.f, gsl, w * 64);
         __syncthreads();
         if (tid < 256) {
             float cp = hc1f[256 + tid];
@@ -628,72 +834,6 @@
         }
         acc = red64(acc);
         if (tid == 0) out[b] = fabsf(acc + pb[0]);
-    }
-}
-
-extern "C" __global__ void repack16b(const float* __restrict__ wihe0,
-                                     const float* __restrict__ wihe1,
-                                     const float* __restrict__ whhe,
-                                     const float* __restrict__ wihd0,
-                                     const float* __restrict__ wihd1,
-                                     const float* __restrict__ whhd,
-                                     const float* __restrict__ aw1,
-                                     const float* __restrict__ dw1,
-                                     __half* __restrict__ ws) {
-    int idx = blockIdx.x * blockDim.x + threadIdx.x;
-    if (idx >= TOT_H) return;
-    int o = idx; float v;
-    if (o < 32768) {
-        int j = o >> 9, p = o & 511;
-        int q = p >> 5, r = p & 31, c = r >> 3, e = r & 7;
-        int k = 8 * q + 128 * c + e;
-        v = aw1[j * 576 + k];
-        ws[OFF_RA + o] = __float2half_rn(v); return;
-    }
-    o -= 32768;
-    if (o < 393216) {
-        int j = o / 384, p = o - j * 384;
-        int q = p / 24, r = p - q * 24, c = r >> 3, e = r & 7;
-        int k = 8 * q + 128 * c + e;
-        v = (k < 64) ? wihe0[j * 64 + k] : (k < 320 ? whhe[j * 256 + (k - 64)] : 0.0f);
-        ws[OFF_RE0 + o] = __float2half_rn(v); return;
-    }
-    o -= 393216;
-    if (o < 524288) {
-        int j = o >> 9, p = o & 511;
-        int q = p >> 5, r = p & 31, c = r >> 3, e = r & 7;
-        int k = 8 * q + 128 * c + e;
-        v = (k < 256) ? wihe1[j * 256 + k] : whhe[262144 + j * 256 + (k - 256)];
-        ws[OFF_RE1 + o] = __float2half_rn(v); return;
-    }
-    o -= 524288;
-    if (o < 131072) {
-        int j = o >> 9, p = o & 511;
-        int q = p >> 5, r = p & 31, c = r >> 3, e = r & 7;
-        int k = 8 * q + 128 * c + e;
-        v = dw1[j * 768 + k];
-        ws[OFF_RDW1 + o] = __float2half_rn(v); return;
-    }
-    o -= 131072;
-    if (o < 524288) {
-        int j = o >> 9, p = o & 511;
-        int q = p >> 5, r = p & 31, c = r >> 3, e = r & 7;
-        int k = 8 * q + 128 * c + e;
-        v = (k < 256) ? wihd0[j * 257 + k] : whhd[j * 256 + (k - 256)];
-        ws[OFF_RD0 + o] = __float2half_rn(v); return;
-    }
-    o -= 524288;
-    if (o < 1024) {
-        v = wihd0[o * 257 + 256];
-        ws[OFF_RDT + o] = __float2half_rn(v); return;
-    }
-    o -= 1024;
-    {
-        int j = o >> 9, p = o & 511;
-        int q = p >> 5, r = p & 31, c = r >> 3, e = r & 7;
-        int k = 8 * q + 128 * c + e;
-        v = (k < 256) ? wihd1[j * 256 + k] : whhd[262144 + j * 256 + (k - 256)];
-        ws[OFF_RD1 + o] = __float2half_rn(v);
     }
 }
 
@@ -721,33 +861,33 @@
     const float* pb    = (const float*)d_in[18];
     float* out = (float*)d_out;
 
-    const size_t EX0 = TOT_H / 2;
+    const size_t EX0 = TOT_H2 / 2;
     const size_t H0X = EX0;
     const size_t H1X = EX0 + 32768;
     const size_t HCX = EX0 + 98304;
     const size_t CTR = EX0 + 131072;
-    const size_t NEED6 = (CTR + 1024) * sizeof(float);
-
-    if (ws_size >= NEED6) {
+    const size_t NEED8 = (CTR + 1024) * sizeof(float);
+
+    if (ws_size >= NEED8) {
         float* ws32 = (float*)d_ws;
         __half* wsh = (__half*)d_ws;
         hipMemsetAsync((char*)d_ws + CTR * sizeof(float), 0, 4096, stream);
-        repack16b<<<(TOT_H + 255) / 256, 256, 0, stream>>>(
+        repack16c<<<(TOT_H2 + 255) / 256, 256, 0, stream>>>(
             wihe0, wihe1, whhe, wihd0, wihd1, whhd, aw1, dw1, wsh);
-        const int smem = M_TOT * 4;
-        hipFuncSetAttribute((const void*)attn_lstm_v6,
+        const int smem = V8_TOT * 4;
+        hipFuncSetAttribute((const void*)attn_lstm_v8,
                             hipFuncAttributeMaxDynamicSharedMemorySize, smem);
-        attn_lstm_v6<<<256, NT, smem, stream>>>(
+        attn_lstm_v8<<<512, NT8, smem, stream>>>(
             inp, wsh, ws32 + H0X, ws32 + H1X, ws32 + HCX,
             (unsigned*)(ws32 + CTR),
             bihe, bhhe, bihd, bhhd,
-            aw1, ab1, aw2, dw1, db1, dw2, pw, pb, out);
+            aw1, ab1, aw2, db1, dw2, pw, pb, out);
         return;
     }
 
-    if (ws_size >= (size_t)TOT_H * sizeof(__half)) {
+    if (ws_size >= (size_t)TOT_H2 * sizeof(__half)) {
         __half* wsh = (__half*)d_ws;
-        repack16b<<<(TOT_H + 255) / 256, 256, 0, stream>>>(
+        repack16c<<<(TOT_H2 + 255) / 256, 256, 0, stream>>>(
             wihe0, wihe1, whhe, wihd0, wihd1, whhd, aw1, dw1, wsh);
         const int smem = L_TOT * 4;
         hipFuncSetAttribute((const void*)attn_lstm_v5,
```
